# Performance work log

Hardware: AMD Instinct MI355X
Metric: run time of the kernel (lower is better)

Reference implementation:

```python
import jax, jax.numpy as jnp
import numpy as np

N_EMBD = 1024
N_HEAD = 16
LN_EPS = 1e-5

def setup_inputs() -> dict:
    key = jax.random.key(0)
    ks = jax.random.split(key, 12)
    B, T, C = 2, 2048, N_EMBD
    s = lambda k, shape, scale=0.02: (jax.random.normal(k, shape, dtype=jnp.float32) * scale)
    return {
        "x": jax.random.normal(ks[0], (B, T, C), dtype=jnp.float32),
        "ln1_g": jnp.ones((C,), jnp.float32),
        "ln1_b": jnp.zeros((C,), jnp.float32),
        "W_attn": s(ks[1], (C, 3 * C)),
        "b_attn": jnp.zeros((3 * C,), jnp.float32),
        "W_o": s(ks[2], (C, C)),
        "b_o": jnp.zeros((C,), jnp.float32),
        "ln2_g": jnp.ones((C,), jnp.float32),
        "ln2_b": jnp.zeros((C,), jnp.float32),
        "W_fc": s(ks[3], (C, 4 * C)),
        "b_fc": jnp.zeros((4 * C,), jnp.float32),
        "W_fc2": s(ks[4], (4 * C, C)),
        "b_fc2": jnp.zeros((C,), jnp.float32),
    }

def _layernorm(x, g, b):
    mu = jnp.mean(x, axis=-1, keepdims=True)
    var = jnp.mean(jnp.square(x - mu), axis=-1, keepdims=True)
    return (x - mu) * jax.lax.rsqrt(var + LN_EPS) * g + b

def reference(x, ln1_g, ln1_b, W_attn, b_attn, W_o, b_o, ln2_g, ln2_b, W_fc, b_fc, W_fc2, b_fc2):
    B, T, C = x.shape
    H, D = N_HEAD, C // N_HEAD
    # ---- attention branch (use_cache=False: T_total == T, causal mask) ----
    h = _layernorm(x, ln1_g, ln1_b)
    qkv = h @ W_attn + b_attn                       # [B,T,3C]
    q, k, v = jnp.split(qkv, 3, axis=-1)
    q = q.reshape(B, T, H, D).transpose(0, 2, 1, 3)  # [B,H,T,D]
    k = k.reshape(B, T, H, D).transpose(0, 2, 1, 3)
    v = v.reshape(B, T, H, D).transpose(0, 2, 1, 3)
    w = jnp.einsum('bhqd,bhkd->bhqk', q, k) / jnp.sqrt(jnp.float32(D))  # [B,H,T,T]
    causal = jnp.tril(jnp.ones((T, T), dtype=bool))
    w = jnp.where(causal, w, jnp.float32(-jnp.inf))
    w = jax.nn.softmax(w, axis=-1)
    y = jnp.einsum('bhqk,bhkd->bhqd', w, v)          # [B,H,T,D]
    y = y.transpose(0, 2, 1, 3).reshape(B, T, C)
    x = x + (y @ W_o + b_o)
    # ---- MLP branch ----
    h2 = _layernorm(x, ln2_g, ln2_b)
    h2 = jax.nn.gelu(h2 @ W_fc + b_fc, approximate=True)  # tanh approx, matches nn.GELU('tanh')
    x = x + (h2 @ W_fc2 + b_fc2)
    return x
```

## Files before the change

kernel.cpp:

```cpp
#include <hip/hip_runtime.h>


typedef unsigned short u16;
typedef unsigned int u32;
typedef __attribute__((ext_vector_type(8))) short v8s;
typedef __attribute__((ext_vector_type(4))) float v4f;

#define GAS __attribute__((address_space(1)))
#define LAS __attribute__((address_space(3)))

__device__ __forceinline__ u16 f2bf(float f) {
  u32 u = __float_as_uint(f);
  u = (u + 0x7FFF + ((u >> 16) & 1)) >> 16;
  return (u16)u;
}
__device__ __forceinline__ u32 f2bf2(float lo, float hi) {
  u32 r;
  asm("v_cvt_pk_bf16_f32 %0, %1, %2" : "=v"(r) : "v"(lo), "v"(hi));
  return r;
}
__device__ __forceinline__ float exp2g(float x) {
  return __builtin_amdgcn_exp2f(x);
}
__device__ __forceinline__ float bf2f(u16 h) {
  return __uint_as_float(((u32)h) << 16);
}
__device__ __forceinline__ float fast_tanh(float x) {
  return 1.f - 2.f / (1.f + __expf(2.f * x));
}

__global__ __launch_bounds__(256)
void wtrans(const float* __restrict__ W, u16* __restrict__ Wt, int K, int N) {
  __shared__ float tile[32][33];
  const int n0 = blockIdx.x << 5, k0 = blockIdx.y << 5;
  const int r = threadIdx.x >> 5, c = threadIdx.x & 31;
#pragma unroll
  for (int i = 0; i < 4; ++i)
    tile[r + 8 * i][c] = W[(size_t)(k0 + r + 8 * i) * N + n0 + c];
  __syncthreads();
#pragma unroll
  for (int i = 0; i < 4; ++i)
    Wt[(size_t)(n0 + r + 8 * i) * K + k0 + c] = f2bf(tile[c][r + 8 * i]);
}

__global__ __launch_bounds__(256)
void ln_bf16(const float* __restrict__ x, const float* __restrict__ g,
             const float* __restrict__ be, u16* __restrict__ out) {
  constexpr int C = 1024;
  const int row = blockIdx.x, t = threadIdx.x;
  const float4 v = ((const float4*)(x + (size_t)row * C))[t];
  float s = v.x + v.y + v.z + v.w;
#pragma unroll
  for (int m = 32; m >= 1; m >>= 1) s += __shfl_xor(s, m);
  __shared__ float red[4], red2[4];
  if ((t & 63) == 0) red[t >> 6] = s;
  __syncthreads();
  const float mu = (red[0] + red[1] + red[2] + red[3]) * (1.f / C);
  const float dx = v.x - mu, dy = v.y - mu, dz = v.z - mu, dw = v.w - mu;
  float s2 = dx * dx + dy * dy + dz * dz + dw * dw;
#pragma unroll
  for (int m = 32; m >= 1; m >>= 1) s2 += __shfl_xor(s2, m);
  if ((t & 63) == 0) red2[t >> 6] = s2;
  __syncthreads();
  const float var = (red2[0] + red2[1] + red2[2] + red2[3]) * (1.f / C);
  const float rs = rsqrtf(var + 1e-5f);
  const int c = t << 2;
  uint2 pk;
  pk.x = f2bf2(dx * rs * g[c + 0] + be[c + 0], dy * rs * g[c + 1] + be[c + 1]);
  pk.y = f2bf2(dz * rs * g[c + 2] + be[c + 2], dw * rs * g[c + 3] + be[c + 3]);
  *(uint2*)(out + (size_t)row * C + c) = pk;
}

template <int EPI, int REMAP>
__global__ __launch_bounds__(256)
void gemm_bt_p(const u16* __restrict__ A, const u16* __restrict__ Bt,
               const float* __restrict__ bias, const float* __restrict__ res,
               void* __restrict__ outp, int M, int N, int K) {
  __shared__ u16 As[3][128 * 32];
  __shared__ u16 Bs[3][128 * 32];
  const int tid = threadIdx.x;
  const int wave = tid >> 6, lane = tid & 63;
  int bx, by;
  if constexpr (REMAP) {
    const int wg = blockIdx.y * (int)gridDim.x + blockIdx.x;
    const int xcd = wg & 7;
    const int seq = wg >> 3;
    bx = seq & 7;
    by = ((seq >> 3) << 3) + xcd;
  } else {
    bx = blockIdx.x;
    by = blockIdx.y;
  }
  const int m0 = by << 7, n0 = bx << 7;

  v4f acc[4][4];
  const v4f vz = {0.f, 0.f, 0.f, 0.f};
#pragma unroll
  for (int i = 0; i < 4; ++i)
#pragma unroll
    for (int j = 0; j < 4; ++j) acc[i][j] = vz;

  const int wm = (wave >> 1) << 6, wn = (wave & 1) << 6;
  const int sr = lane >> 2;
  const int sc = (((lane & 3) ^ ((lane >> 4) & 3)) << 3);
  const int fr = lane & 15;
  const int fg = lane >> 4;
  const int c0 = wave << 1;

  const u16* gA0 = A + (size_t)(m0 + c0 * 16 + sr) * K + sc;
  const u16* gA1 = A + (size_t)(m0 + c0 * 16 + 16 + sr) * K + sc;
  const u16* gB0 = Bt + (size_t)(n0 + c0 * 16 + sr) * K + sc;
  const u16* gB1 = Bt + (size_t)(n0 + c0 * 16 + 16 + sr) * K + sc;
  const int aoff = c0 * 512;

  const u32 asb = (u32)(size_t)(LAS const u16*)&As[0][0];
  const u32 bsb = (u32)(size_t)(LAS const u16*)&Bs[0][0];
  const int cgp = fg ^ ((fr >> 2) & 3);
  const u32 afrag = (u32)(((wm + fr) << 6) + (cgp << 4));
  const u32 bfrag = (u32)(((wn + fr) << 6) + (cgp << 4));

  const int nk = K >> 5;

#define P128_ISSUE(t, bf)                                                        \
  do {                                                                           \
    const int k0_ = (t) << 5;                                                    \
    __builtin_amdgcn_global_load_lds((GAS const u32*)(gA0 + k0_),                \
                                     (LAS u32*)(As[bf] + aoff), 16, 0, 0);       \
    __builtin_amdgcn_global_load_lds((GAS const u32*)(gA1 + k0_),                \
                                     (LAS u32*)(As[bf] + aoff + 512), 16, 0, 0); \
    __builtin_amdgcn_global_load_lds((GAS const u32*)(gB0 + k0_),                \
                                     (LAS u32*)(Bs[bf] + aoff), 16, 0, 0);       \
    __builtin_amdgcn_global_load_lds((GAS const u32*)(gB1 + k0_),                \
                                     (LAS u32*)(Bs[bf] + aoff + 512), 16, 0, 0); \
  } while (0)

  auto ldfr = [&](int buf, v8s (&a)[4], v8s (&b)[4]) __attribute__((always_inline)) {
    const u32 ab = asb + ((u32)buf << 13) + afrag;
    const u32 bb = bsb + ((u32)buf << 13) + bfrag;
    asm volatile("ds_read_b128 %0, %1 offset:0"    : "=v"(a[0]) : "v"(ab));
    asm volatile("ds_read_b128 %0, %1 offset:1024" : "=v"(a[1]) : "v"(ab));
    asm volatile("ds_read_b128 %0, %1 offset:2048" : "=v"(a[2]) : "v"(ab));
    asm volatile("ds_read_b128 %0, %1 offset:3072" : "=v"(a[3]) : "v"(ab));
    asm volatile("ds_read_b128 %0, %1 offset:0"    : "=v"(b[0]) : "v"(bb));
    asm volatile("ds_read_b128 %0, %1 offset:1024" : "=v"(b[1]) : "v"(bb));
    asm volatile("ds_read_b128 %0, %1 offset:2048" : "=v"(b[2]) : "v"(bb));
    asm volatile("ds_read_b128 %0, %1 offset:3072" : "=v"(b[3]) : "v"(bb));
  };
  auto wait8 = [&](v8s (&a)[4], v8s (&b)[4]) __attribute__((always_inline)) {
    asm volatile("s_waitcnt lgkmcnt(0)"
                 : "+v"(a[0]), "+v"(a[1]), "+v"(a[2]), "+v"(a[3]),
                   "+v"(b[0]), "+v"(b[1]), "+v"(b[2]), "+v"(b[3])
                 :
                 : "memory");
  };
  auto mfma16 = [&](v8s (&a)[4], v8s (&b)[4]) __attribute__((always_inline)) {
#pragma unroll
    for (int i = 0; i < 4; ++i)
#pragma unroll
      for (int j = 0; j < 4; ++j)
        acc[i][j] = __builtin_amdgcn_mfma_f32_16x16x32_bf16(a[i], b[j], acc[i][j], 0, 0, 0);
  };

  v8s aX[4], bX[4], aY[4], bY[4];

  P128_ISSUE(0, 0);
  P128_ISSUE(1, 1);
  P128_ISSUE(2, 2);
  asm volatile("s_waitcnt vmcnt(8)" ::: "memory");
  __builtin_amdgcn_s_barrier();
  ldfr(0, aX, bX);
  wait8(aX, bX);

  int br = 1, bi = 0;
  for (int kt = 0; kt < nk - 2; kt += 2) {
    asm volatile("s_waitcnt vmcnt(4)" ::: "memory");
    __builtin_amdgcn_s_barrier();
    ldfr(br, aY, bY);
    if (kt + 3 < nk) P128_ISSUE(kt + 3, bi);
    __builtin_amdgcn_sched_barrier(0);
    mfma16(aX, bX);
    wait8(aY, bY);
    br = (br == 2) ? 0 : br + 1;
    bi = (bi == 2) ? 0 : bi + 1;
    asm volatile("s_waitcnt vmcnt(4)" ::: "memory");
    __builtin_amdgcn_s_barrier();
    ldfr(br, aX, bX);
    if (kt + 4 < nk) P128_ISSUE(kt + 4, bi);
    __builtin_amdgcn_sched_barrier(0);
    mfma16(aY, bY);
    wait8(aX, bX);
    br = (br == 2) ? 0 : br + 1;
    bi = (bi == 2) ? 0 : bi + 1;
  }
  asm volatile("s_waitcnt vmcnt(0)" ::: "memory");
  __builtin_amdgcn_s_barrier();
  ldfr(br, aY, bY);
  __builtin_amdgcn_sched_barrier(0);
  mfma16(aX, bX);
  wait8(aY, bY);
  mfma16(aY, bY);
#undef P128_ISSUE

  const int er = (lane >> 4) << 2;
#pragma unroll
  for (int mi = 0; mi < 4; ++mi) {
#pragma unroll
    for (int ni = 0; ni < 4; ++ni) {
      const int col = n0 + wn + ni * 16 + fr;
      const float bcol = bias[col];
#pragma unroll
      for (int r = 0; r < 4; ++r) {
        const int row = m0 + wm + mi * 16 + er + r;
        float v = acc[mi][ni][r] + bcol;
        if constexpr (EPI == 1) {
          const float t = fast_tanh(0.7978845608028654f * (v + 0.044715f * v * v * v));
          v = 0.5f * v * (1.f + t);
        }
        if constexpr (EPI == 2) {
          v += res[(size_t)row * N + col];
          ((float*)outp)[(size_t)row * N + col] = v;
        } else {
          ((u16*)outp)[(size_t)row * N + col] = f2bf(v);
        }
      }
    }
  }
}

template <int EPI>
__global__ __launch_bounds__(256)
void gemm_bt_n64(const u16* __restrict__ A, const u16* __restrict__ Bt,
                 const float* __restrict__ bias, const float* __restrict__ res,
                 void* __restrict__ outp, int M, int N, int K) {
  __shared__ u16 As[4][128 * 32];
  __shared__ u16 Bs[4][64 * 32];
  const int tid = threadIdx.x;
  const int wave = tid >> 6, lane = tid & 63;
  const int m0 = blockIdx.y << 7, n0 = blockIdx.x << 6;

  v4f acc[4][2];
  const v4f vz = {0.f, 0.f, 0.f, 0.f};
#pragma unroll
  for (int i = 0; i < 4; ++i)
#pragma unroll
    for (int j = 0; j < 2; ++j) acc[i][j] = vz;

  const int wm = (wave >> 1) << 6, wn = (wave & 1) << 5;
  const int sr = lane >> 2;
  const int sc = (((lane & 3) ^ ((lane >> 4) & 3)) << 3);
  const int fr = lane & 15;
  const int fg = lane >> 4;

  const u16* gA0 = A + (size_t)(m0 + wave * 32 + sr) * K + sc;
  const u16* gA1 = A + (size_t)(m0 + wave * 32 + 16 + sr) * K + sc;
  const u16* gB0 = Bt + (size_t)(n0 + wave * 16 + sr) * K + sc;
  const int aoff = wave * 1024;
  const int boff = wave * 512;

  const u32 asb = (u32)(size_t)(LAS const u16*)&As[0][0];
  const u32 bsb = (u32)(size_t)(LAS const u16*)&Bs[0][0];
  const int cgp = fg ^ ((fr >> 2) & 3);
  const u32 afrag = (u32)(((wm + fr) << 6) + (cgp << 4));
  const u32 bfrag = (u32)(((wn + fr) << 6) + (cgp << 4));

  const int nk = K >> 5;

#define N64_ISSUE(t, bf)                                                      \
  do {                                                                        \
    const int k0_ = (t) << 5;                                                 \
    __builtin_amdgcn_global_load_lds((GAS const u32*)(gA0 + k0_),             \
                                     (LAS u32*)(As[bf] + aoff), 16, 0, 0);    \
    __builtin_amdgcn_global_load_lds((GAS const u32*)(gA1 + k0_),             \
                                     (LAS u32*)(As[bf] + aoff + 512), 16, 0, 0); \
    __builtin_amdgcn_global_load_lds((GAS const u32*)(gB0 + k0_),             \
                                     (LAS u32*)(Bs[bf] + boff), 16, 0, 0);    \
  } while (0)

  N64_ISSUE(0, 0);
  N64_ISSUE(1, 1);
  N64_ISSUE(2, 2);

  auto compute = [&](int kt) __attribute__((always_inline)) {
    const u32 ab = asb + ((u32)(kt & 3) << 13) + afrag;
    const u32 bb = bsb + ((u32)(kt & 3) << 12) + bfrag;
    v8s a0, a1, a2, a3, b0, b1;
    asm volatile("ds_read_b128 %0, %1 offset:0"    : "=v"(a0) : "v"(ab));
    asm volatile("ds_read_b128 %0, %1 offset:1024" : "=v"(a1) : "v"(ab));
    asm volatile("ds_read_b128 %0, %1 offset:2048" : "=v"(a2) : "v"(ab));
    asm volatile("ds_read_b128 %0, %1 offset:3072" : "=v"(a3) : "v"(ab));
    asm volatile("ds_read_b128 %0, %1 offset:0"    : "=v"(b0) : "v"(bb));
    asm volatile("ds_read_b128 %0, %1 offset:1024" : "=v"(b1) : "v"(bb));
    asm volatile("s_waitcnt lgkmcnt(0)"
                 : "+v"(a0), "+v"(a1), "+v"(a2), "+v"(a3), "+v"(b0), "+v"(b1)
                 :
                 : "memory");
    acc[0][0] = __builtin_amdgcn_mfma_f32_16x16x32_bf16(a0, b0, acc[0][0], 0, 0, 0);
    acc[0][1] = __builtin_amdgcn_mfma_f32_16x16x32_bf16(a0, b1, acc[0][1], 0, 0, 0);
    acc[1][0] = __builtin_amdgcn_mfma_f32_16x16x32_bf16(a1, b0, acc[1][0], 0, 0, 0);
    acc[1][1] = __builtin_amdgcn_mfma_f32_16x16x32_bf16(a1, b1, acc[1][1], 0, 0, 0);
    acc[2][0] = __builtin_amdgcn_mfma_f32_16x16x32_bf16(a2, b0, acc[2][0], 0, 0, 0);
    acc[2][1] = __builtin_amdgcn_mfma_f32_16x16x32_bf16(a2, b1, acc[2][1], 0, 0, 0);
    acc[3][0] = __builtin_amdgcn_mfma_f32_16x16x32_bf16(a3, b0, acc[3][0], 0, 0, 0);
    acc[3][1] = __builtin_amdgcn_mfma_f32_16x16x32_bf16(a3, b1, acc[3][1], 0, 0, 0);
  };

  for (int kt = 0; kt < nk - 2; ++kt) {
    asm volatile("s_waitcnt vmcnt(6)" ::: "memory");
    __builtin_amdgcn_s_barrier();
    if (kt + 3 < nk) N64_ISSUE(kt + 3, (kt + 3) & 3);
    compute(kt);
  }
  asm volatile("s_waitcnt vmcnt(3)" ::: "memory");
  __builtin_amdgcn_s_barrier();
  compute(nk - 2);
  asm volatile("s_waitcnt vmcnt(0)" ::: "memory");
  __builtin_amdgcn_s_barrier();
  compute(nk - 1);
#undef N64_ISSUE

  const int er = (lane >> 4) << 2;
#pragma unroll
  for (int mi = 0; mi < 4; ++mi) {
#pragma unroll
    for (int ni = 0; ni < 2; ++ni) {
      const int col = n0 + wn + ni * 16 + fr;
      const float bcol = bias[col];
#pragma unroll
      for (int r = 0; r < 4; ++r) {
        const int row = m0 + wm + mi * 16 + er + r;
        float v = acc[mi][ni][r] + bcol;
        if constexpr (EPI == 1) {
          const float t = fast_tanh(0.7978845608028654f * (v + 0.044715f * v * v * v));
          v = 0.5f * v * (1.f + t);
        }
        if constexpr (EPI == 2) {
          v += res[(size_t)row * N + col];
          ((float*)outp)[(size_t)row * N + col] = v;
        } else {
          ((u16*)outp)[(size_t)row * N + col] = f2bf(v);
        }
      }
    }
  }
}

__global__ __launch_bounds__(256)
void transpose_v(const u16* __restrict__ qkv, u16* __restrict__ Vt) {
  __shared__ u16 tile[64][65];
  const int t0 = blockIdx.x << 6;
  const int bh = blockIdx.y;
  const int b = bh >> 4, h = bh & 15;
  const int r4 = threadIdx.x >> 6, c = threadIdx.x & 63;
#pragma unroll
  for (int i = 0; i < 16; ++i) {
    const int r = r4 * 16 + i;
    tile[r][c] = qkv[(size_t)(b * 2048 + t0 + r) * 3072 + 2048 + h * 64 + c];
  }
  __syncthreads();
#pragma unroll
  for (int i = 0; i < 16; ++i) {
    const int d = r4 * 16 + i;
    Vt[(size_t)bh * 64 * 2048 + (size_t)d * 2048 + t0 + c] = tile[c][d];
  }
}

constexpr int PSTR = 88;
constexpr float ATT_SC = 0.18033688011112042f;

template <bool MASKED>
__device__ __forceinline__ void soft16(
    const v4f (&st)[4], float (&e)[4][4], v4f (&ot)[4],
    float& m_i, float& l_i, const int kb, const int qrow,
    const int fr, const int fg) {
  const int q = qrow + fr;
#pragma unroll
  for (int ks = 0; ks < 4; ++ks) {
    const v4f sv = st[ks] * ATT_SC;
#pragma unroll
    for (int r = 0; r < 4; ++r) {
      float v = sv[r];
      if (MASKED) v = (kb + ks * 16 + fg * 4 + r <= q) ? v : -1e30f;
      e[ks][r] = v;
    }
  }
  float mk0 = fmaxf(fmaxf(e[0][0], e[0][1]), fmaxf(e[0][2], e[0][3]));
  float mk1 = fmaxf(fmaxf(e[1][0], e[1][1]), fmaxf(e[1][2], e[1][3]));
  float mk2 = fmaxf(fmaxf(e[2][0], e[2][1]), fmaxf(e[2][2], e[2][3]));
  float mk3 = fmaxf(fmaxf(e[3][0], e[3][1]), fmaxf(e[3][2], e[3][3]));
  float mt = fmaxf(fmaxf(mk0, mk1), fmaxf(mk2, mk3));
  mt = fmaxf(mt, __shfl_xor(mt, 16));
  mt = fmaxf(mt, __shfl_xor(mt, 32));
  if (__any(mt > m_i)) {
    const float m_new = fmaxf(m_i, mt);
    const float alpha = exp2g(m_i - m_new);
    m_i = m_new;
    l_i *= alpha;
#pragma unroll
    for (int ds = 0; ds < 4; ++ds) ot[ds] *= alpha;
  }
#pragma unroll
  for (int ks = 0; ks < 4; ++ks)
#pragma unroll
    for (int r = 0; r < 4; ++r) e[ks][r] = exp2g(e[ks][r] - m_i);
  float s0 = (e[0][0] + e[0][1]) + (e[0][2] + e[0][3]);
  float s1 = (e[1][0] + e[1][1]) + (e[1][2] + e[1][3]);
  float s2 = (e[2][0] + e[2][1]) + (e[2][2] + e[2][3]);
  float s3 = (e[3][0] + e[3][1]) + (e[3][2] + e[3][3]);
  float ls = (s0 + s1) + (s2 + s3);
  ls += __shfl_xor(ls, 16);
  ls += __shfl_xor(ls, 32);
  l_i += ls;
}

__device__ __forceinline__ void pstore(const float (&e)[4][4],
                                       u16* __restrict__ pw,
                                       const int fr, const int fg) {
#pragma unroll
  for (int ks = 0; ks < 4; ++ks) {
    uint2 pk;
    pk.x = f2bf2(e[ks][0], e[ks][1]);
    pk.y = f2bf2(e[ks][2], e[ks][3]);
    *(uint2*)&pw[fr * PSTR + ks * 16 + fg * 4] = pk;
  }
}

__device__ __forceinline__ void pvacc(const v8s (&vfr)[4][2],
                                      const u16* __restrict__ pw,
                                      v4f (&ot)[4], const int fr, const int fg) {
  const v8s pf0 = *(const v8s*)&pw[fr * PSTR + fg * 8];
  const v8s pf1 = *(const v8s*)&pw[fr * PSTR + 32 + fg * 8];
  __builtin_amdgcn_s_setprio(1);
#pragma unroll
  for (int ds = 0; ds < 4; ++ds) {
    ot[ds] = __builtin_amdgcn_mfma_f32_16x16x32_bf16(vfr[ds][0], pf0, ot[ds], 0, 0, 0);
    ot[ds] = __builtin_amdgcn_mfma_f32_16x16x32_bf16(vfr[ds][1], pf1, ot[ds], 0, 0, 0);
  }
  __builtin_amdgcn_s_setprio(0);
}

template <bool MASKED>
__device__ __forceinline__ void attn_sub(
    const v8s (&kf)[4][2], const v8s (&vfr)[4][2], const v8s (&qf)[2],
    v4f (&ot)[4], float& m_i, float& l_i, u16* __restrict__ pw,
    const int kb, const int qrow, const int fr, const int fg) {
  const v4f vz = {0.f, 0.f, 0.f, 0.f};
  v4f st[4];
  __builtin_amdgcn_s_setprio(1);
#pragma unroll
  for (int ks = 0; ks < 4; ++ks) {
    st[ks] = vz;
    st[ks] = __builtin_amdgcn_mfma_f32_16x16x32_bf16(kf[ks][0], qf[0], st[ks], 0, 0, 0);
    st[ks] = __builtin_amdgcn_mfma_f32_16x16x32_bf16(kf[ks][1], qf[1], st[ks], 0, 0, 0);
  }
  __builtin_amdgcn_s_setprio(0);
  float e[4][4];
  soft16<MASKED>(st, e, ot, m_i, l_i, kb, qrow, fr, fg);
  pstore(e, pw, fr, fg);
  pvacc(vfr, pw, ot, fr, fg);
}

template <bool MASKA>
__device__ __forceinline__ void attn_sub_pair(
    const v8s (&kf)[4][2], const v8s (&vfr)[4][2],
    const v8s (&qfA)[2], const v8s (&qfB)[2],
    v4f (&otA)[4], v4f (&otB)[4],
    float& mA, float& lA, float& mB, float& lB,
    u16* __restrict__ pwA, u16* __restrict__ pwB,
    const int kb, const int rowA, const int rowB, const int fr, const int fg) {
  const v4f vz = {0.f, 0.f, 0.f, 0.f};
  v4f stA[4], stB[4];
  __builtin_amdgcn_s_setprio(1);
#pragma unroll
  for (int ks = 0; ks < 4; ++ks) {
    stA[ks] = vz;
    stA[ks] = __builtin_amdgcn_mfma_f32_16x16x32_bf16(kf[ks][0], qfA[0], stA[ks], 0, 0, 0);
    stA[ks] = __builtin_amdgcn_mfma_f32_16x16x32_bf16(kf[ks][1], qfA[1], stA[ks], 0, 0, 0);
  }
#pragma unroll
  for (int ks = 0; ks < 4; ++ks) {
    stB[ks] = vz;
    stB[ks] = __builtin_amdgcn_mfma_f32_16x16x32_bf16(kf[ks][0], qfB[0], stB[ks], 0, 0, 0);
    stB[ks] = __builtin_amdgcn_mfma_f32_16x16x32_bf16(kf[ks][1], qfB[1], stB[ks], 0, 0, 0);
  }
  __builtin_amdgcn_s_setprio(0);
  float eA[4][4];
  soft16<MASKA>(stA, eA, otA, mA, lA, kb, rowA, fr, fg);
  pstore(eA, pwA, fr, fg);
  float eB[4][4];
  soft16<false>(stB, eB, otB, mB, lB, kb, rowB, fr, fg);
  pvacc(vfr, pwA, otA, fr, fg);
  pstore(eB, pwB, fr, fg);
  pvacc(vfr, pwB, otB, fr, fg);
}

__global__ __launch_bounds__(256)
void attn_kernel(const u16* __restrict__ qkv, const u16* __restrict__ Vt,
                 u16* __restrict__ y) {
  constexpr int T = 2048, D = 64, C = 1024, QS = 3072;
  __shared__ alignas(16) u16 Ktile[2][64 * 64];
  __shared__ alignas(16) u16 Vtile[2][64 * 64];
  __shared__ alignas(16) u16 Pw[8][16 * PSTR];

  const int tid = threadIdx.x, wave = tid >> 6, lane = tid & 63;
  const int fr = lane & 15, fg = lane >> 4;
  const int wg = blockIdx.y * 16 + blockIdx.x;
  const int xcd = wg & 7, seq = wg >> 3;
  const int bh = ((seq & 3) << 3) + xcd;
  const int ta = seq >> 2, tb = 31 - ta;
  const int b = bh >> 4, h = bh & 15;
  const u16* qkvb = qkv + (size_t)b * T * QS + h * 64;
  const u16* Kg = qkvb + 1024;
  const u16* Vh = Vt + (size_t)bh * D * T;
  u16* pwA = &Pw[wave][0];
  u16* pwB = &Pw[4 + wave][0];

  const int rowA = ta * 64 + wave * 16;
  const int rowB = tb * 64 + wave * 16;

  v8s qfA[2], qfB[2];
#pragma unroll
  for (int dh = 0; dh < 2; ++dh) {
    qfA[dh] = *(const v8s*)&qkvb[(size_t)(rowA + fr) * QS + dh * 32 + fg * 8];
    qfB[dh] = *(const v8s*)&qkvb[(size_t)(rowB + fr) * QS + dh * 32 + fg * 8];
  }

  const v4f vz = {0.f, 0.f, 0.f, 0.f};
  v4f otA[4], otB[4];
#pragma unroll
  for (int ds = 0; ds < 4; ++ds) { otA[ds] = vz; otB[ds] = vz; }
  float mA = -1e30f, lA = 0.f, mB = -1e30f, lB = 0.f;

  const int srow = lane >> 3;
  const int sg0 = lane & 7;

  const int nt = tb + 1;
  {
#pragma unroll
    for (int cc = 0; cc < 2; ++cc) {
      const int r0 = wave * 16 + cc * 8;
      const int rr = r0 + srow;
      const int gg = sg0 ^ (rr & 7);
      __builtin_amdgcn_global_load_lds(
          (GAS const u32*)(Kg + (size_t)rr * QS + gg * 8),
          (LAS u32*)(Ktile[0] + r0 * 64), 16, 0, 0);
      __builtin_amdgcn_global_load_lds(
          (GAS const u32*)(Vh + (size_t)rr * T + gg * 8),
          (LAS u32*)(Vtile[0] + r0 * 64), 16, 0, 0);
    }
  }
  for (int kt = 0; kt < nt; ++kt) {
    __syncthreads();
    if (kt + 1 < nt) {
      const int kb1 = (kt + 1) << 6;
      const int nb = (kt + 1) & 1;
#pragma unroll
      for (int cc = 0; cc < 2; ++cc) {
        const int r0 = wave * 16 + cc * 8;
        const int rr = r0 + srow;
        const int gg = sg0 ^ (rr & 7);
        __builtin_amdgcn_global_load_lds(
            (GAS const u32*)(Kg + (size_t)(kb1 + rr) * QS + gg * 8),
            (LAS u32*)(Ktile[nb] + r0 * 64), 16, 0, 0);
        __builtin_amdgcn_global_load_lds(
            (GAS const u32*)(Vh + (size_t)rr * T + kb1 + gg * 8),
            (LAS u32*)(Vtile[nb] + r0 * 64), 16, 0, 0);
      }
    }
    const u16* Kt = Ktile[kt & 1];
    const u16* Vi = Vtile[kt & 1];
    const int kb = kt << 6;
    const int swz = fr & 7;
    v8s kf[4][2], vfr[4][2];
#pragma unroll
    for (int ks = 0; ks < 4; ++ks) {
      const int rr = ks * 16 + fr;
      kf[ks][0] = *(const v8s*)&Kt[rr * 64 + ((0 + fg) ^ swz) * 8];
      kf[ks][1] = *(const v8s*)&Kt[rr * 64 + ((4 + fg) ^ swz) * 8];
      vfr[ks][0] = *(const v8s*)&Vi[rr * 64 + ((0 + fg) ^ swz) * 8];
      vfr[ks][1] = *(const v8s*)&Vi[rr * 64 + ((4 + fg) ^ swz) * 8];
    }
    if (kt < ta) {
      attn_sub_pair<false>(kf, vfr, qfA, qfB, otA, otB, mA, lA, mB, lB,
                           pwA, pwB, kb, rowA, rowB, fr, fg);
    } else if (kt == ta) {
      attn_sub_pair<true>(kf, vfr, qfA, qfB, otA, otB, mA, lA, mB, lB,
                          pwA, pwB, kb, rowA, rowB, fr, fg);
    } else if (kt < tb) {
      attn_sub<false>(kf, vfr, qfB, otB, mB, lB, pwB, kb, rowB, fr, fg);
    } else {
      attn_sub<true>(kf, vfr, qfB, otB, mB, lB, pwB, kb, rowB, fr, fg);
    }
  }

  const float invA = 1.f / lA, invB = 1.f / lB;
#pragma unroll
  for (int ds = 0; ds < 4; ++ds) {
    uint2 pa, pb;
    pa.x = f2bf2(otA[ds][0] * invA, otA[ds][1] * invA);
    pa.y = f2bf2(otA[ds][2] * invA, otA[ds][3] * invA);
    pb.x = f2bf2(otB[ds][0] * invB, otB[ds][1] * invB);
    pb.y = f2bf2(otB[ds][2] * invB, otB[ds][3] * invB);
    *(uint2*)&y[(size_t)(b * T + rowA + fr) * C + h * D + ds * 16 + fg * 4] = pa;
    *(uint2*)&y[(size_t)(b * T + rowB + fr) * C + h * D + ds * 16 + fg * 4] = pb;
  }
}

extern "C" void kernel_launch(void* const* d_in, const int* in_sizes, int n_in,
                              void* d_out, int out_size, void* d_ws, size_t ws_size,
                              hipStream_t stream) {
  const float* x      = (const float*)d_in[0];
  const float* ln1_g  = (const float*)d_in[1];
  const float* ln1_b  = (const float*)d_in[2];
  const float* W_attn = (const float*)d_in[3];
  const float* b_attn = (const float*)d_in[4];
  const float* W_o    = (const float*)d_in[5];
  const float* b_o    = (const float*)d_in[6];
  const float* ln2_g  = (const float*)d_in[7];
  const float* ln2_b  = (const float*)d_in[8];
  const float* W_fc   = (const float*)d_in[9];
  const float* b_fc   = (const float*)d_in[10];
  const float* W_fc2  = (const float*)d_in[11];
  const float* b_fc2  = (const float*)d_in[12];
  float* out = (float*)d_out;
  char* ws = (char*)d_ws;

  const size_t MB = 1u << 20;
  u16* Wattn_t = (u16*)(ws + 0 * MB);
  u16* Wo_t    = (u16*)(ws + 6 * MB);
  u16* Wfc_t   = (u16*)(ws + 8 * MB);
  u16* Wfc2_t  = (u16*)(ws + 16 * MB);
  float* x1    = (float*)(ws + 24 * MB);
  u16* h1      = (u16*)(ws + 40 * MB);
  u16* qkv     = (u16*)(ws + 48 * MB);
  u16* Vt      = (u16*)(ws + 88 * MB);
  u16* yb      = (u16*)(ws + 40 * MB);
  u16* h2      = (u16*)(ws + 48 * MB);
  u16* ab      = (u16*)(ws + 56 * MB);

  wtrans<<<dim3(3072 / 32, 1024 / 32), 256, 0, stream>>>(W_attn, Wattn_t, 1024, 3072);
  wtrans<<<dim3(1024 / 32, 1024 / 32), 256, 0, stream>>>(W_o, Wo_t, 1024, 1024);
  wtrans<<<dim3(4096 / 32, 1024 / 32), 256, 0, stream>>>(W_fc, Wfc_t, 1024, 4096);
  wtrans<<<dim3(1024 / 32, 4096 / 32), 256, 0, stream>>>(W_fc2, Wfc2_t, 4096, 1024);

  ln_bf16<<<4096, 256, 0, stream>>>(x, ln1_g, ln1_b, h1);
  gemm_bt_p<0, 0><<<dim3(3072 / 128, 4096 / 128), 256, 0, stream>>>(
      h1, Wattn_t, b_attn, nullptr, qkv, 4096, 3072, 1024);
  transpose_v<<<dim3(2048 / 64, 32), 256, 0, stream>>>(qkv, Vt);
  attn_kernel<<<dim3(16, 32), 256, 0, stream>>>(qkv, Vt, yb);
  gemm_bt_n64<2><<<dim3(1024 / 64, 4096 / 128), 256, 0, stream>>>(
      yb, Wo_t, b_o, x, x1, 4096, 1024, 1024);
  ln_bf16<<<4096, 256, 0, stream>>>(x1, ln2_g, ln2_b, h2);
  gemm_bt_p<1, 0><<<dim3(4096 / 128, 4096 / 128), 256, 0, stream>>>(
      h2, Wfc_t, b_fc, nullptr, ab, 4096, 4096, 1024);
  gemm_bt_p<2, 1><<<dim3(1024 / 128, 4096 / 128), 256, 0, stream>>>(
      ab, Wfc2_t, b_fc2, x1, out, 4096, 1024, 4096);
}
```

Before: 338.3 us.

## Add 256x256-tile 512-thread GEMM with 4-stage LDS pipeline for QKV and FC

Adds a new bf16 GEMM kernel with a 256x256 output tile, 8 waves and a 4-buffer global_load_lds pipeline that keeps three k-steps in flight. Each wave computes a 128x64 sub-tile with a larger MFMA accumulator block. The kernel replaces the 128x128 GEMM for the QKV projection and the FC+GELU projection. The aim is more operand reuse per LDS and global byte and less load traffic. In exchange, the grids shrink to 192 and 256 workgroups, and the 128 KB LDS footprint allows about one block per CU. That risks underfilling the device, especially for QKV. The epilogue also writes scalar, non-vectorized elements.

```diff
diff --git a/kernel.cpp b/kernel.cpp
--- a/kernel.cpp
+++ b/kernel.cpp
@@ -69,6 +69,141 @@
   pk.x = f2bf2(dx * rs * g[c + 0] + be[c + 0], dy * rs * g[c + 1] + be[c + 1]);
   pk.y = f2bf2(dz * rs * g[c + 2] + be[c + 2], dw * rs * g[c + 3] + be[c + 3]);
   *(uint2*)(out + (size_t)row * C + c) = pk;
+}
+
+template <int EPI>
+__global__ __launch_bounds__(512, 2)
+void gemm_bt_p256(const u16* __restrict__ A, const u16* __restrict__ Bt,
+                  const float* __restrict__ bias, const float* __restrict__ res,
+                  void* __restrict__ outp, int M, int N, int K) {
+  __shared__ u16 As[4][256 * 32];
+  __shared__ u16 Bs[4][256 * 32];
+  const int tid = threadIdx.x;
+  const int wave = tid >> 6, lane = tid & 63;
+  const int m0 = blockIdx.y << 8, n0 = blockIdx.x << 8;
+
+  v4f acc[8][4];
+  const v4f vz = {0.f, 0.f, 0.f, 0.f};
+#pragma unroll
+  for (int i = 0; i < 8; ++i)
+#pragma unroll
+    for (int j = 0; j < 4; ++j) acc[i][j] = vz;
+
+  const int wm = (wave >> 2) << 7;
+  const int wn = (wave & 3) << 6;
+  const int fr = lane & 15;
+  const int fg = lane >> 4;
+
+  const int sr = tid >> 2;
+  const int sc = (((tid & 3) ^ ((tid >> 4) & 3)) << 3);
+  const u16* gA0 = A + (size_t)(m0 + sr) * K + sc;
+  const u16* gA1 = gA0 + (size_t)128 * K;
+  const u16* gB0 = Bt + (size_t)(n0 + sr) * K + sc;
+  const u16* gB1 = gB0 + (size_t)128 * K;
+  const int aoff = wave * 512;
+
+  const u32 asb = (u32)(size_t)(LAS const u16*)&As[0][0];
+  const u32 bsb = (u32)(size_t)(LAS const u16*)&Bs[0][0];
+  const int cgp = fg ^ ((fr >> 2) & 3);
+  const u32 afrag = (u32)(((wm + fr) << 6) + (cgp << 4));
+  const u32 bfrag = (u32)(((wn + fr) << 6) + (cgp << 4));
+
+  const int nk = K >> 5;
+
+#define P256_ISSUE(t, bf)                                                         \
+  do {                                                                            \
+    const int k0_ = (t) << 5;                                                     \
+    __builtin_amdgcn_global_load_lds((GAS const u32*)(gA0 + k0_),                 \
+                                     (LAS u32*)(As[bf] + aoff), 16, 0, 0);        \
+    __builtin_amdgcn_global_load_lds((GAS const u32*)(gA1 + k0_),                 \
+                                     (LAS u32*)(As[bf] + aoff + 4096), 16, 0, 0); \
+    __builtin_amdgcn_global_load_lds((GAS const u32*)(gB0 + k0_),                 \
+                                     (LAS u32*)(Bs[bf] + aoff), 16, 0, 0);        \
+    __builtin_amdgcn_global_load_lds((GAS const u32*)(gB1 + k0_),                 \
+                                     (LAS u32*)(Bs[bf] + aoff + 4096), 16, 0, 0); \
+  } while (0)
+
+  v8s a[8], b[4];
+  auto ldfr = [&](int buf) __attribute__((always_inline)) {
+    const u32 ab = asb + ((u32)buf << 14) + afrag;
+    const u32 bb = bsb + ((u32)buf << 14) + bfrag;
+    asm volatile("ds_read_b128 %0, %1 offset:0"    : "=v"(a[0]) : "v"(ab));
+    asm volatile("ds_read_b128 %0, %1 offset:1024" : "=v"(a[1]) : "v"(ab));
+    asm volatile("ds_read_b128 %0, %1 offset:2048" : "=v"(a[2]) : "v"(ab));
+    asm volatile("ds_read_b128 %0, %1 offset:3072" : "=v"(a[3]) : "v"(ab));
+    asm volatile("ds_read_b128 %0, %1 offset:4096" : "=v"(a[4]) : "v"(ab));
+    asm volatile("ds_read_b128 %0, %1 offset:5120" : "=v"(a[5]) : "v"(ab));
+    asm volatile("ds_read_b128 %0, %1 offset:6144" : "=v"(a[6]) : "v"(ab));
+    asm volatile("ds_read_b128 %0, %1 offset:7168" : "=v"(a[7]) : "v"(ab));
+    asm volatile("ds_read_b128 %0, %1 offset:0"    : "=v"(b[0]) : "v"(bb));
+    asm volatile("ds_read_b128 %0, %1 offset:1024" : "=v"(b[1]) : "v"(bb));
+    asm volatile("ds_read_b128 %0, %1 offset:2048" : "=v"(b[2]) : "v"(bb));
+    asm volatile("ds_read_b128 %0, %1 offset:3072" : "=v"(b[3]) : "v"(bb));
+    asm volatile("s_waitcnt lgkmcnt(0)"
+                 : "+v"(a[0]), "+v"(a[1]), "+v"(a[2]), "+v"(a[3]),
+                   "+v"(a[4]), "+v"(a[5]), "+v"(a[6]), "+v"(a[7]),
+                   "+v"(b[0]), "+v"(b[1]), "+v"(b[2]), "+v"(b[3])
+                 :
+                 : "memory");
+  };
+  auto mfma32 = [&]() __attribute__((always_inline)) {
+#pragma unroll
+    for (int i = 0; i < 8; ++i)
+#pragma unroll
+      for (int j = 0; j < 4; ++j)
+        acc[i][j] = __builtin_amdgcn_mfma_f32_16x16x32_bf16(a[i], b[j], acc[i][j], 0, 0, 0);
+  };
+
+  P256_ISSUE(0, 0);
+  P256_ISSUE(1, 1);
+  P256_ISSUE(2, 2);
+
+  for (int kt = 0; kt < nk - 3; ++kt) {
+    asm volatile("s_waitcnt vmcnt(8)" ::: "memory");
+    __builtin_amdgcn_s_barrier();
+    P256_ISSUE(kt + 3, (kt + 3) & 3);
+    __builtin_amdgcn_sched_barrier(0);
+    ldfr(kt & 3);
+    mfma32();
+  }
+  asm volatile("s_waitcnt vmcnt(8)" ::: "memory");
+  __builtin_amdgcn_s_barrier();
+  ldfr((nk - 3) & 3);
+  mfma32();
+  asm volatile("s_waitcnt vmcnt(4)" ::: "memory");
+  __builtin_amdgcn_s_barrier();
+  ldfr((nk - 2) & 3);
+  mfma32();
+  asm volatile("s_waitcnt vmcnt(0)" ::: "memory");
+  __builtin_amdgcn_s_barrier();
+  ldfr((nk - 1) & 3);
+  mfma32();
+#undef P256_ISSUE
+
+  const int er = (lane >> 4) << 2;
+#pragma unroll
+  for (int mi = 0; mi < 8; ++mi) {
+#pragma unroll
+    for (int ni = 0; ni < 4; ++ni) {
+      const int col = n0 + wn + ni * 16 + fr;
+      const float bcol = bias[col];
+#pragma unroll
+      for (int r = 0; r < 4; ++r) {
+        const int row = m0 + wm + mi * 16 + er + r;
+        float v = acc[mi][ni][r] + bcol;
+        if constexpr (EPI == 1) {
+          const float t = fast_tanh(0.7978845608028654f * (v + 0.044715f * v * v * v));
+          v = 0.5f * v * (1.f + t);
+        }
+        if constexpr (EPI == 2) {
+          v += res[(size_t)row * N + col];
+          ((float*)outp)[(size_t)row * N + col] = v;
+        } else {
+          ((u16*)outp)[(size_t)row * N + col] = f2bf(v);
+        }
+      }
+    }
+  }
 }
 
 template <int EPI, int REMAP>
@@ -643,14 +778,14 @@
   wtrans<<<dim3(1024 / 32, 4096 / 32), 256, 0, stream>>>(W_fc2, Wfc2_t, 4096, 1024);
 
   ln_bf16<<<4096, 256, 0, stream>>>(x, ln1_g, ln1_b, h1);
-  gemm_bt_p<0, 0><<<dim3(3072 / 128, 4096 / 128), 256, 0, stream>>>(
+  gemm_bt_p256<0><<<dim3(3072 / 256, 4096 / 256), 512, 0, stream>>>(
       h1, Wattn_t, b_attn, nullptr, qkv, 4096, 3072, 1024);
   transpose_v<<<dim3(2048 / 64, 32), 256, 0, stream>>>(qkv, Vt);
   attn_kernel<<<dim3(16, 32), 256, 0, stream>>>(qkv, Vt, yb);
   gemm_bt_n64<2><<<dim3(1024 / 64, 4096 / 128), 256, 0, stream>>>(
       yb, Wo_t, b_o, x, x1, 4096, 1024, 1024);
   ln_bf16<<<4096, 256, 0, stream>>>(x1, ln2_g, ln2_b, h2);
-  gemm_bt_p<1, 0><<<dim3(4096 / 128, 4096 / 128), 256, 0, stream>>>(
+  gemm_bt_p256<1><<<dim3(4096 / 256, 4096 / 256), 512, 0, stream>>>(
       h2, Wfc_t, b_fc, nullptr, ab, 4096, 4096, 1024);
   gemm_bt_p<2, 1><<<dim3(1024 / 128, 4096 / 128), 256, 0, stream>>>(
       ab, Wfc2_t, b_fc2, x1, out, 4096, 1024, 4096);
```

New measurement: 352.1 us. 1.04x slower.
